# Performance work log

Hardware: AMD Instinct MI355X
Metric: run time of the kernel (lower is better)

Reference implementation:

```python
import jax, jax.numpy as jnp
import numpy as np

H, W, C_IN, HID, OUT = 96, 96, 3, 16, 10
BETA, THRESH = 0.9, 1.0


def _spherical_adjacency(h, w):
    # self + 8 toroidal neighbors, row-normalized (every row sums to 9 here)
    n = h * w
    ys, xs = np.meshgrid(np.arange(h), np.arange(w), indexing='ij')
    src = (ys * w + xs).ravel()
    adj = np.zeros((n, n), dtype=np.float32)
    for dy, dx in [(0, 0), (-1, 0), (1, 0), (0, -1), (0, 1),
                   (-1, -1), (-1, 1), (1, -1), (1, 1)]:
        dst = (((ys + dy) % h) * w + ((xs + dx) % w)).ravel()
        adj[src, dst] = 1.0
    adj /= np.maximum(adj.sum(axis=-1, keepdims=True), 1.0)
    return jnp.asarray(adj)

ADJ = _spherical_adjacency(H, W)  # [N, N], N = H*W


@jax.custom_vjp
def spike(u):
    return (u > 0).astype(u.dtype)

def _spike_fwd(u):
    return spike(u), u

def _spike_bwd(u, g):
    k = 25.0  # superspike surrogate slope
    return (g / (1.0 + k * jnp.abs(u)) ** 2,)

spike.defvjp(_spike_fwd, _spike_bwd)


def setup_inputs() -> dict:
    key = jax.random.key(0)
    ks = jax.random.split(key, 3)
    T, B = 8, 2
    return {
        'x_seq': jax.random.normal(ks[0], (T, B, H, W, C_IN), jnp.float32),
        'w_proj': jax.random.normal(ks[1], (C_IN, HID), jnp.float32) / np.sqrt(C_IN),
        'b_proj': jnp.zeros((HID,), jnp.float32),
        'w_head': jax.random.normal(ks[2], (HID, OUT), jnp.float32) / np.sqrt(HID),
        'b_head': jnp.zeros((OUT,), jnp.float32),
    }


def reference(x_seq, w_proj, b_proj, w_head, b_head):
    T, B = x_seq.shape[0], x_seq.shape[1]
    N = H * W
    v0 = jnp.zeros((B, H, W, HID), x_seq.dtype)  # LIF membrane state

    def step(v, x_t):
        # 1x1 conv == per-pixel linear projection
        z = jnp.einsum('bhwc,cd->bhwd', x_t, w_proj) + b_proj
        flat = z.reshape(B, N, HID)
        agg = jnp.einsum('nm,bmc->bnc', ADJ, flat)  # adjacency aggregation
        smooth_t = jnp.mean(jnp.abs(agg - flat))
        z_g = agg.reshape(B, H, W, HID)
        # LIF: integrate, threshold, soft reset
        v_new = BETA * v + z_g
        s_t = spike(v_new - THRESH)
        v_new = v_new - s_t * THRESH
        logits_t = jnp.mean(s_t, axis=(1, 2)) @ w_head + b_head
        return v_new, (logits_t, jnp.mean(s_t), smooth_t)

    _, (logits_seq, sr_seq, smooth_seq) = jax.lax.scan(step, v0, x_seq)
    out = jnp.mean(logits_seq, axis=0)  # 'mean' readout over time
    return out, logits_seq, jnp.mean(sr_seq)[None], jnp.mean(smooth_seq)
```

## Files before the change

### kernel.cpp

```cpp
#include <hip/hip_runtime.h>

#define HH 96
#define WW 96
#define NPX (HH*WW)
#define HID 16
#define OUTC 10
#define TT 8
#define BB 2
#define BETA 0.9f

#define THREADS 384
#define NBLK (BB*HH)

#define SM_BASE (TT*4*NBLK)
#define DENOM 2359296.0f

#define SLABW 292
#define VPAD 97

__device__ __forceinline__ float4 proj4(float xa, float xb, float xc,
                                        const float* w0, const float* w1, const float* w2)
{
  float4 r;
  r.x = fmaf(xc, w2[0], fmaf(xb, w1[0], xa*w0[0]));
  r.y = fmaf(xc, w2[1], fmaf(xb, w1[1], xa*w0[1]));
  r.z = fmaf(xc, w2[2], fmaf(xb, w1[2], xa*w0[2]));
  r.w = fmaf(xc, w2[3], fmaf(xb, w1[3], xa*w0[3]));
  return r;
}

__global__ __launch_bounds__(THREADS)
void snn_main(const float* __restrict__ x,
              const float* __restrict__ wproj,
              const float* __restrict__ bproj,
              float* __restrict__ ws)
{
  __shared__ float4 xraw4[24*73];
  __shared__ float4 vbuf[TT*VPAD];
  __shared__ unsigned cslot[TT][6][4];
  __shared__ float  smslot[6];

  const int row  = blockIdx.x;
  const int b    = blockIdx.y;
  const int blk  = b*HH + row;
  const int tid  = threadIdx.x;
  const int lane = tid & 63;
  const int wv   = tid >> 6;
  const int cg   = tid & 3;
  const int col  = tid >> 2;

  float w0[4], w1[4], w2[4], bp[4];
#pragma unroll
  for (int j = 0; j < 4; ++j) {
    w0[j] = wproj[0*HID + cg*4 + j];
    w1[j] = wproj[1*HID + cg*4 + j];
    w2[j] = wproj[2*HID + cg*4 + j];
    bp[j] = bproj[cg*4 + j];
  }

#pragma unroll
  for (int i = 0; i < 5; ++i) {
    int idx = tid + THREADS*i;
    if (idx < 1728) {
      int s = idx / 72;
      int q = idx - s*72;
      int t = s / 3;
      int g = s - t*3;
      int rr = row + g - 1;
      rr = (rr < 0) ? rr + HH : (rr >= HH ? rr - HH : rr);
      const float4* src = (const float4*)(x + ((size_t)(t*BB + b)*NPX + (size_t)rr*WW)*3);
      xraw4[s*73 + q] = src[q];
    }
  }
  __syncthreads();
  const float* xr = (const float*)xraw4;

#pragma unroll
  for (int i = 0; i < 2; ++i) {
    int t = cg*2 + i;
    int base = t*3*SLABW + col*3;
    float s0 = xr[base    ] + xr[base + SLABW    ] + xr[base + 2*SLABW    ];
    float s1 = xr[base + 1] + xr[base + SLABW + 1] + xr[base + 2*SLABW + 1];
    float s2 = xr[base + 2] + xr[base + SLABW + 2] + xr[base + 2*SLABW + 2];
    vbuf[t*VPAD + col] = make_float4(s0, s1, s2, 0.f);
  }
  __syncthreads();

  const int cl = (col == 0)    ? (WW-1) : (col-1);
  const int cr = (col == WW-1) ? 0      : (col+1);
  float4 v = make_float4(0.f, 0.f, 0.f, 0.f);
  float sm = 0.f;
  unsigned packw[TT];
  const float inv9 = 1.0f/9.0f;
  const unsigned long long fm = 0x1111111111111111ULL << cg;

#pragma unroll
  for (int t = 0; t < TT; ++t) {
    float4 a0 = vbuf[t*VPAD + cl];
    float4 a1 = vbuf[t*VPAD + col];
    float4 a2 = vbuf[t*VPAD + cr];
    float bx = a0.x + a1.x + a2.x;
    float by = a0.y + a1.y + a2.y;
    float bz = a0.z + a1.z + a2.z;
    int cb = (t*3 + 1)*SLABW + col*3;
    float xc0 = xr[cb], xc1 = xr[cb+1], xc2 = xr[cb+2];
    float4 pb = proj4(bx, by, bz, w0, w1, w2);
    float4 pz = proj4(xc0, xc1, xc2, w0, w1, w2);
    float ax = pb.x*inv9, ay = pb.y*inv9, az = pb.z*inv9, aw = pb.w*inv9;
    sm += fabsf(ax - pz.x) + fabsf(ay - pz.y) + fabsf(az - pz.z) + fabsf(aw - pz.w);
    float vx = fmaf(BETA, v.x, ax + bp[0]);
    float vy = fmaf(BETA, v.y, ay + bp[1]);
    float vz = fmaf(BETA, v.z, az + bp[2]);
    float vw = fmaf(BETA, v.w, aw + bp[3]);
    bool b0 = vx > 1.0f, b1 = vy > 1.0f, b2 = vz > 1.0f, b3 = vw > 1.0f;
    unsigned long long m0 = __ballot(b0);
    unsigned long long m1 = __ballot(b1);
    unsigned long long m2 = __ballot(b2);
    unsigned long long m3 = __ballot(b3);
    unsigned c0 = (unsigned)__popcll(m0 & fm);
    unsigned c1 = (unsigned)__popcll(m1 & fm);
    unsigned c2 = (unsigned)__popcll(m2 & fm);
    unsigned c3 = (unsigned)__popcll(m3 & fm);
    packw[t] = c0 | (c1 << 8) | (c2 << 16) | (c3 << 24);
    v.x = vx - (b0 ? 1.0f : 0.0f);
    v.y = vy - (b1 ? 1.0f : 0.0f);
    v.z = vz - (b2 ? 1.0f : 0.0f);
    v.w = vw - (b3 ? 1.0f : 0.0f);
  }

  if (lane < 4) {
#pragma unroll
    for (int t = 0; t < TT; ++t)
      cslot[t][wv][lane] = packw[t];
  }
#pragma unroll
  for (int off = 1; off < 64; off <<= 1)
    sm += __shfl_xor(sm, off);
  if (lane == 0) smslot[wv] = sm;
  __syncthreads();

  unsigned* wsu = (unsigned*)ws;
  if (tid < 32) {
    int t = tid >> 2, c4 = tid & 3;
    unsigned s = cslot[t][0][c4] + cslot[t][1][c4] + cslot[t][2][c4]
               + cslot[t][3][c4] + cslot[t][4][c4] + cslot[t][5][c4];
    wsu[(t*4 + c4)*NBLK + blk] = s;
  }
  if (tid == 0)
    ws[SM_BASE + blk] = smslot[0]+smslot[1]+smslot[2]+smslot[3]+smslot[4]+smslot[5];
}

__global__ __launch_bounds__(320)
void snn_final(const float* __restrict__ ws,
               const float* __restrict__ whead,
               const float* __restrict__ bhead,
               float* __restrict__ out)
{
  __shared__ float cnt_s[TT][BB][HID];
  const int tid  = threadIdx.x;

  float smacc = 0.f;
  if (tid >= 256) {
    int i = tid - 256;
    smacc = ws[SM_BASE + i] + ws[SM_BASE + 64 + i] + ws[SM_BASE + 128 + i];
  }

  if (tid < 256) {
    const unsigned* wsu = (const unsigned*)ws;
    int slot = tid >> 3, sub = tid & 7;
    const uint4* src = (const uint4*)(wsu + slot*NBLK) + sub*6;
    unsigned c0 = 0, c1 = 0, c2 = 0, c3 = 0;
#pragma unroll
    for (int q = 0; q < 6; ++q) {
      uint4 a = src[q];
      unsigned p0 = a.x + a.y, p1 = a.z + a.w;
      c0 += (p0 & 0xffu)        + (p1 & 0xffu);
      c1 += ((p0 >> 8) & 0xffu) + ((p1 >> 8) & 0xffu);
      c2 += ((p0 >> 16) & 0xffu)+ ((p1 >> 16) & 0xffu);
      c3 += (p0 >> 24)          + (p1 >> 24);
    }
    c0 += __shfl_xor(c0, 1); c1 += __shfl_xor(c1, 1);
    c2 += __shfl_xor(c2, 1); c3 += __shfl_xor(c3, 1);
    c0 += __shfl_xor(c0, 2); c1 += __shfl_xor(c1, 2);
    c2 += __shfl_xor(c2, 2); c3 += __shfl_xor(c3, 2);
    if ((sub & 3) == 0) {
      int half = sub >> 2;
      int t = slot >> 2, cg = slot & 3;
      cnt_s[t][half][cg*4 + 0] = (float)c0;
      cnt_s[t][half][cg*4 + 1] = (float)c1;
      cnt_s[t][half][cg*4 + 2] = (float)c2;
      cnt_s[t][half][cg*4 + 3] = (float)c3;
    }
  }
  __syncthreads();

  if (tid < 160) {
    int t  = tid / (BB*OUTC);
    int r  = tid - t*(BB*OUTC);
    int bq = r / OUTC;
    int o  = r - bq*OUTC;
    float acc = bhead[o];
#pragma unroll
    for (int d = 0; d < HID; ++d)
      acc = fmaf(cnt_s[t][bq][d] * (1.0f/9216.0f), whead[d*OUTC + o], acc);
    out[20 + tid] = acc;
  } else if (tid < 180) {
    int r  = tid - 160;
    int bq = r / OUTC;
    int o  = r - bq*OUTC;
    float acc = bhead[o];
#pragma unroll
    for (int d = 0; d < HID; ++d) {
      float s = 0.f;
#pragma unroll
      for (int t = 0; t < TT; ++t) s += cnt_s[t][bq][d];
      acc = fmaf(s * (1.0f/(9216.0f*TT)), whead[d*OUTC + o], acc);
    }
    out[r] = acc;
  } else if (tid >= 192 && tid < 256) {
    int i = tid - 192;
    const float* cf = &cnt_s[0][0][0];
    float s = cf[i] + cf[i + 64] + cf[i + 128] + cf[i + 192];
#pragma unroll
    for (int off = 1; off < 64; off <<= 1)
      s += __shfl_xor(s, off);
    if (i == 0) out[180] = s / DENOM;
  } else if (tid >= 256) {
#pragma unroll
    for (int off = 1; off < 64; off <<= 1)
      smacc += __shfl_xor(smacc, off);
    if (tid == 256) out[181] = smacc / DENOM;
  }
}

extern "C" void kernel_launch(void* const* d_in, const int* in_sizes, int n_in,
                              void* d_out, int out_size, void* d_ws, size_t ws_size,
                              hipStream_t stream)
{
  const float* x     = (const float*)d_in[0];
  const float* wproj = (const float*)d_in[1];
  const float* bproj = (const float*)d_in[2];
  const float* whead = (const float*)d_in[3];
  const float* bhead = (const float*)d_in[4];
  float* out = (float*)d_out;
  float* ws  = (float*)d_ws;

  dim3 grid(HH, BB);
  snn_main<<<grid, dim3(THREADS), 0, stream>>>(x, wproj, bproj, ws);
  snn_final<<<1, dim3(320), 0, stream>>>(ws, whead, bhead, out);
}
```

Before: 13.00 us.

## Fuse main and final kernels via cooperative launch with grid sync

Merges the two kernels into one cooperative kernel. After writing per-block partials, all blocks do a grid-wide sync and block (0,0) performs the final reduction and head projection. This removes the second kernel launch and its gap, but cooperative launch and grid sync have their own overhead, which may cost as much as the launch it replaces at this small runtime.

```diff
diff --git a/kernel.cpp b/kernel.cpp
--- a/kernel.cpp
+++ b/kernel.cpp
@@ -1,4 +1,7 @@
 #include <hip/hip_runtime.h>
+#include <hip/hip_cooperative_groups.h>
+
+namespace cg = cooperative_groups;
 
 #define HH 96
 #define WW 96
@@ -30,15 +33,19 @@
 }
 
 __global__ __launch_bounds__(THREADS)
-void snn_main(const float* __restrict__ x,
+void snn_coop(const float* __restrict__ x,
               const float* __restrict__ wproj,
               const float* __restrict__ bproj,
-              float* __restrict__ ws)
+              const float* __restrict__ whead,
+              const float* __restrict__ bhead,
+              float* __restrict__ ws,
+              float* __restrict__ out)
 {
   __shared__ float4 xraw4[24*73];
   __shared__ float4 vbuf[TT*VPAD];
   __shared__ unsigned cslot[TT][6][4];
   __shared__ float  smslot[6];
+  __shared__ float  cnt_s[TT][BB][HID];
 
   const int row  = blockIdx.x;
   const int b    = blockIdx.y;
@@ -148,27 +155,20 @@
   }
   if (tid == 0)
     ws[SM_BASE + blk] = smslot[0]+smslot[1]+smslot[2]+smslot[3]+smslot[4]+smslot[5];
-}
-
-__global__ __launch_bounds__(320)
-void snn_final(const float* __restrict__ ws,
-               const float* __restrict__ whead,
-               const float* __restrict__ bhead,
-               float* __restrict__ out)
-{
-  __shared__ float cnt_s[TT][BB][HID];
-  const int tid  = threadIdx.x;
+
+  cg::this_grid().sync();
+
+  if (row != 0 || b != 0) return;
 
   float smacc = 0.f;
-  if (tid >= 256) {
+  if (tid >= 256 && tid < 320) {
     int i = tid - 256;
     smacc = ws[SM_BASE + i] + ws[SM_BASE + 64 + i] + ws[SM_BASE + 128 + i];
   }
 
   if (tid < 256) {
-    const unsigned* wsu = (const unsigned*)ws;
     int slot = tid >> 3, sub = tid & 7;
-    const uint4* src = (const uint4*)(wsu + slot*NBLK) + sub*6;
+    const uint4* src = (const uint4*)((const unsigned*)ws + slot*NBLK) + sub*6;
     unsigned c0 = 0, c1 = 0, c2 = 0, c3 = 0;
 #pragma unroll
     for (int q = 0; q < 6; ++q) {
@@ -185,11 +185,11 @@
     c2 += __shfl_xor(c2, 2); c3 += __shfl_xor(c3, 2);
     if ((sub & 3) == 0) {
       int half = sub >> 2;
-      int t = slot >> 2, cg = slot & 3;
-      cnt_s[t][half][cg*4 + 0] = (float)c0;
-      cnt_s[t][half][cg*4 + 1] = (float)c1;
-      cnt_s[t][half][cg*4 + 2] = (float)c2;
-      cnt_s[t][half][cg*4 + 3] = (float)c3;
+      int t = slot >> 2, c4 = slot & 3;
+      cnt_s[t][half][c4*4 + 0] = (float)c0;
+      cnt_s[t][half][c4*4 + 1] = (float)c1;
+      cnt_s[t][half][c4*4 + 2] = (float)c2;
+      cnt_s[t][half][c4*4 + 3] = (float)c3;
     }
   }
   __syncthreads();
@@ -225,7 +225,7 @@
     for (int off = 1; off < 64; off <<= 1)
       s += __shfl_xor(s, off);
     if (i == 0) out[180] = s / DENOM;
-  } else if (tid >= 256) {
+  } else if (tid >= 256 && tid < 320) {
 #pragma unroll
     for (int off = 1; off < 64; off <<= 1)
       smacc += __shfl_xor(smacc, off);
@@ -245,7 +245,8 @@
   float* out = (float*)d_out;
   float* ws  = (float*)d_ws;
 
-  dim3 grid(HH, BB);
-  snn_main<<<grid, dim3(THREADS), 0, stream>>>(x, wproj, bproj, ws);
-  snn_final<<<1, dim3(320), 0, stream>>>(ws, whead, bhead, out);
+  void* args[] = { (void*)&x, (void*)&wproj, (void*)&bproj,
+                   (void*)&whead, (void*)&bhead, (void*)&ws, (void*)&out };
+  dim3 grid(HH, BB), block(THREADS);
+  (void)hipLaunchCooperativeKernel((const void*)snn_coop, grid, block, args, 0, stream);
 }
```

Result: slower. 45.75 us (+252.0%).

## Split hidden channels across eight threads per column, doubling block size

Applied to the files above, without the earlier changes.

Doubles the threads per block to 768 so each thread handles 2 hidden channels instead of 4. The per-thread work in the time loop (projections, ballots, LIF updates) is halved, aiming to cut the serial latency of each block in what is a small, latency-bound grid. The trade-off is more wavefronts per block, a larger cross-wave reduction over 12 wave slots, and a repacking of counts into the existing 8-bit-per-channel workspace layout.

```diff
diff --git a/kernel.cpp b/kernel.cpp
--- a/kernel.cpp
+++ b/kernel.cpp
@@ -9,7 +9,7 @@
 #define BB 2
 #define BETA 0.9f
 
-#define THREADS 384
+#define THREADS 768
 #define NBLK (BB*HH)
 
 #define SM_BASE (TT*4*NBLK)
@@ -17,17 +17,6 @@
 
 #define SLABW 292
 #define VPAD 97
-
-__device__ __forceinline__ float4 proj4(float xa, float xb, float xc,
-                                        const float* w0, const float* w1, const float* w2)
-{
-  float4 r;
-  r.x = fmaf(xc, w2[0], fmaf(xb, w1[0], xa*w0[0]));
-  r.y = fmaf(xc, w2[1], fmaf(xb, w1[1], xa*w0[1]));
-  r.z = fmaf(xc, w2[2], fmaf(xb, w1[2], xa*w0[2]));
-  r.w = fmaf(xc, w2[3], fmaf(xb, w1[3], xa*w0[3]));
-  return r;
-}
 
 __global__ __launch_bounds__(THREADS)
 void snn_main(const float* __restrict__ x,
@@ -37,8 +26,8 @@
 {
   __shared__ float4 xraw4[24*73];
   __shared__ float4 vbuf[TT*VPAD];
-  __shared__ unsigned cslot[TT][6][4];
-  __shared__ float  smslot[6];
+  __shared__ unsigned cslot[TT][12][8];
+  __shared__ float  smslot[12];
 
   const int row  = blockIdx.x;
   const int b    = blockIdx.y;
@@ -46,20 +35,20 @@
   const int tid  = threadIdx.x;
   const int lane = tid & 63;
   const int wv   = tid >> 6;
-  const int cg   = tid & 3;
-  const int col  = tid >> 2;
-
-  float w0[4], w1[4], w2[4], bp[4];
-#pragma unroll
-  for (int j = 0; j < 4; ++j) {
-    w0[j] = wproj[0*HID + cg*4 + j];
-    w1[j] = wproj[1*HID + cg*4 + j];
-    w2[j] = wproj[2*HID + cg*4 + j];
-    bp[j] = bproj[cg*4 + j];
-  }
-
-#pragma unroll
-  for (int i = 0; i < 5; ++i) {
+  const int cg2  = tid & 7;
+  const int col  = tid >> 3;
+
+  float w0[2], w1[2], w2[2], bp[2];
+#pragma unroll
+  for (int j = 0; j < 2; ++j) {
+    w0[j] = wproj[0*HID + cg2*2 + j];
+    w1[j] = wproj[1*HID + cg2*2 + j];
+    w2[j] = wproj[2*HID + cg2*2 + j];
+    bp[j] = bproj[cg2*2 + j];
+  }
+
+#pragma unroll
+  for (int i = 0; i < 3; ++i) {
     int idx = tid + THREADS*i;
     if (idx < 1728) {
       int s = idx / 72;
@@ -75,24 +64,24 @@
   __syncthreads();
   const float* xr = (const float*)xraw4;
 
-#pragma unroll
-  for (int i = 0; i < 2; ++i) {
-    int t = cg*2 + i;
-    int base = t*3*SLABW + col*3;
+  {
+    int t = tid & 7;
+    int c = tid >> 3;
+    int base = t*3*SLABW + c*3;
     float s0 = xr[base    ] + xr[base + SLABW    ] + xr[base + 2*SLABW    ];
     float s1 = xr[base + 1] + xr[base + SLABW + 1] + xr[base + 2*SLABW + 1];
     float s2 = xr[base + 2] + xr[base + SLABW + 2] + xr[base + 2*SLABW + 2];
-    vbuf[t*VPAD + col] = make_float4(s0, s1, s2, 0.f);
+    vbuf[t*VPAD + c] = make_float4(s0, s1, s2, 0.f);
   }
   __syncthreads();
 
   const int cl = (col == 0)    ? (WW-1) : (col-1);
   const int cr = (col == WW-1) ? 0      : (col+1);
-  float4 v = make_float4(0.f, 0.f, 0.f, 0.f);
+  float v0 = 0.f, v1 = 0.f;
   float sm = 0.f;
   unsigned packw[TT];
   const float inv9 = 1.0f/9.0f;
-  const unsigned long long fm = 0x1111111111111111ULL << cg;
+  const unsigned long long fm = 0x0101010101010101ULL << cg2;
 
 #pragma unroll
   for (int t = 0; t < TT; ++t) {
@@ -104,31 +93,25 @@
     float bz = a0.z + a1.z + a2.z;
     int cb = (t*3 + 1)*SLABW + col*3;
     float xc0 = xr[cb], xc1 = xr[cb+1], xc2 = xr[cb+2];
-    float4 pb = proj4(bx, by, bz, w0, w1, w2);
-    float4 pz = proj4(xc0, xc1, xc2, w0, w1, w2);
-    float ax = pb.x*inv9, ay = pb.y*inv9, az = pb.z*inv9, aw = pb.w*inv9;
-    sm += fabsf(ax - pz.x) + fabsf(ay - pz.y) + fabsf(az - pz.z) + fabsf(aw - pz.w);
-    float vx = fmaf(BETA, v.x, ax + bp[0]);
-    float vy = fmaf(BETA, v.y, ay + bp[1]);
-    float vz = fmaf(BETA, v.z, az + bp[2]);
-    float vw = fmaf(BETA, v.w, aw + bp[3]);
-    bool b0 = vx > 1.0f, b1 = vy > 1.0f, b2 = vz > 1.0f, b3 = vw > 1.0f;
-    unsigned long long m0 = __ballot(b0);
-    unsigned long long m1 = __ballot(b1);
-    unsigned long long m2 = __ballot(b2);
-    unsigned long long m3 = __ballot(b3);
+    float pb0 = fmaf(bz, w2[0], fmaf(by, w1[0], bx*w0[0]));
+    float pb1 = fmaf(bz, w2[1], fmaf(by, w1[1], bx*w0[1]));
+    float pz0 = fmaf(xc2, w2[0], fmaf(xc1, w1[0], xc0*w0[0]));
+    float pz1 = fmaf(xc2, w2[1], fmaf(xc1, w1[1], xc0*w0[1]));
+    float ag0 = pb0*inv9, ag1 = pb1*inv9;
+    sm += fabsf(ag0 - pz0) + fabsf(ag1 - pz1);
+    float vx = fmaf(BETA, v0, ag0 + bp[0]);
+    float vy = fmaf(BETA, v1, ag1 + bp[1]);
+    bool s0 = vx > 1.0f, s1 = vy > 1.0f;
+    unsigned long long m0 = __ballot(s0);
+    unsigned long long m1 = __ballot(s1);
     unsigned c0 = (unsigned)__popcll(m0 & fm);
     unsigned c1 = (unsigned)__popcll(m1 & fm);
-    unsigned c2 = (unsigned)__popcll(m2 & fm);
-    unsigned c3 = (unsigned)__popcll(m3 & fm);
-    packw[t] = c0 | (c1 << 8) | (c2 << 16) | (c3 << 24);
-    v.x = vx - (b0 ? 1.0f : 0.0f);
-    v.y = vy - (b1 ? 1.0f : 0.0f);
-    v.z = vz - (b2 ? 1.0f : 0.0f);
-    v.w = vw - (b3 ? 1.0f : 0.0f);
-  }
-
-  if (lane < 4) {
+    packw[t] = c0 | (c1 << 8);
+    v0 = vx - (s0 ? 1.0f : 0.0f);
+    v1 = vy - (s1 ? 1.0f : 0.0f);
+  }
+
+  if (lane < 8) {
 #pragma unroll
     for (int t = 0; t < TT; ++t)
       cslot[t][wv][lane] = packw[t];
@@ -142,12 +125,20 @@
   unsigned* wsu = (unsigned*)ws;
   if (tid < 32) {
     int t = tid >> 2, c4 = tid & 3;
-    unsigned s = cslot[t][0][c4] + cslot[t][1][c4] + cslot[t][2][c4]
-               + cslot[t][3][c4] + cslot[t][4][c4] + cslot[t][5][c4];
-    wsu[(t*4 + c4)*NBLK + blk] = s;
-  }
-  if (tid == 0)
-    ws[SM_BASE + blk] = smslot[0]+smslot[1]+smslot[2]+smslot[3]+smslot[4]+smslot[5];
+    unsigned s01 = 0, s23 = 0;
+#pragma unroll
+    for (int w = 0; w < 12; ++w) {
+      s01 += cslot[t][w][c4*2];
+      s23 += cslot[t][w][c4*2 + 1];
+    }
+    wsu[(t*4 + c4)*NBLK + blk] = (s01 & 0xffffu) | ((s23 & 0xffffu) << 16);
+  }
+  if (tid == 0) {
+    float a = 0.f;
+#pragma unroll
+    for (int w = 0; w < 12; ++w) a += smslot[w];
+    ws[SM_BASE + blk] = a;
+  }
 }
 
 __global__ __launch_bounds__(320)
```

New measurement: 12.75 us. Within noise of the previous version (-1.9%).
